# Optimization experiments

Measured on AMD Instinct MI355X. Metric: run time of the kernel, lower is better.

The kernel has to match this reference:

```python
import jax, jax.numpy as jnp
import numpy as np

PCH_SIZE = 8
STRIDE = 3


def setup_inputs() -> dict:
    key = jax.random.key(0)
    x = jax.random.normal(key, (8, 3, 512, 512), dtype=jnp.float32)
    return {"x": x}


def _estimate_noise(x, p=PCH_SIZE, s=STRIDE):
    B = x.shape[0]
    # Extract overlapping patches: [B, C*p*p, Hp, Wp] (NCHW input).
    pch = jax.lax.conv_general_dilated_patches(x, (p, p), (s, s), 'VALID')
    d = pch.shape[1]                       # C*p*p = 192
    pch = pch.reshape(B, d, -1)            # [B, d, num_pch]
    num_pch = pch.shape[-1]
    mu = pch.mean(axis=-1, keepdims=True)
    X = pch - mu
    # Patch covariance: [B, d, d]
    sigma_X = jnp.einsum('bdn,ben->bde', X, X) / num_pch
    sig = jnp.sort(jnp.linalg.eigvalsh(sigma_X), axis=-1)  # [B, d], ascending

    # Vectorized version of the original sequential threshold search.
    # Loop iteration ii = -1..-d uses prefix sig[..., :d+ii] of length L = d-1..0.
    ks = jnp.arange(d)
    L = d - 1 - ks                          # prefix lengths in original loop order
    csum = jnp.cumsum(sig, axis=-1)         # [B, d]
    prefix_sum = jnp.where(L > 0, csum[:, jnp.clip(L - 1, 0, d - 1)], 0.0)  # [B, d]
    tau = prefix_sum / jnp.maximum(L, 1).astype(sig.dtype)                  # [B, d]

    j = jnp.arange(d)
    in_prefix = j[None, :] < L[:, None]     # [K, d] membership of eig j in prefix k
    greater = (sig[:, None, :] > tau[:, :, None]) & in_prefix[None]
    less = (sig[:, None, :] < tau[:, :, None]) & in_prefix[None]
    valid = greater.sum(axis=-1) == less.sum(axis=-1)  # [B, K]

    # First valid iteration in loop order (mirrors the `found` flag).
    idx = jnp.argmax(valid, axis=-1)                    # [B]
    tau_sel = jnp.take_along_axis(tau, idx[:, None], axis=-1)[:, 0]
    return jnp.sqrt(tau_sel)                             # [B]


def reference(x):
    return _estimate_noise(x)
```

## Files before the change

kernel.cpp:

```cpp
#include <hip/hip_runtime.h>
#include <math.h>

#define NB 8
#define NC 3
#define PD 192
#define IMG 512
#define NP 169
#define NPATCH 28561
#define INV_N (1.0f/28561.0f)
#define KST 32

typedef float f4 __attribute__((ext_vector_type(4)));
typedef __bf16 bf16x8 __attribute__((ext_vector_type(8)));
typedef float f32x4 __attribute__((ext_vector_type(4)));

__device__ __forceinline__ float rdlane(float v, int lane) {
  return __uint_as_float(__builtin_amdgcn_readlane(__float_as_uint(v), lane));
}

template<int CTRL, int RM, int BM>
__device__ __forceinline__ float dpp_add(float x) {
  int sh = __builtin_amdgcn_update_dpp(0, __float_as_int(x), CTRL, RM, BM, false);
  return x + __int_as_float(sh);
}
__device__ __forceinline__ float wave_sum(float x) {
  x = dpp_add<0x111, 0xF, 0xF>(x);
  x = dpp_add<0x112, 0xF, 0xF>(x);
  x = dpp_add<0x114, 0xF, 0xF>(x);
  x = dpp_add<0x118, 0xF, 0xF>(x);
  x = dpp_add<0x142, 0xA, 0xF>(x);
  x = dpp_add<0x143, 0xC, 0xF>(x);
  return rdlane(x, 63);
}
__device__ __forceinline__ float row16_sum(float x) {
  x = dpp_add<0x111, 0xF, 0xF>(x);
  x = dpp_add<0x112, 0xF, 0xF>(x);
  x = dpp_add<0x114, 0xF, 0xF>(x);
  x = dpp_add<0x118, 0xF, 0xF>(x);
  return rdlane(x, 15);
}

__device__ __forceinline__ unsigned bfh(float v) {
  unsigned u = __float_as_uint(v);
  return (u + 0x7FFFu + ((u >> 16) & 1u)) >> 16;
}

__global__ __launch_bounds__(512) void cov_gemm_k(const float* __restrict__ x,
                                                  float* __restrict__ partial,
                                                  float* __restrict__ Spart,
                                                  int CH, int chunkSize) {
  int chunk = blockIdx.x % CH;
  int b = blockIdx.x / CH;
  int p0 = chunk * chunkSize;
  int pcount = NPATCH - p0;
  if (pcount > chunkSize) pcount = chunkSize;
  if (pcount < 0) pcount = 0;
  int nkt = (pcount + KST - 1) / KST;
  int pend = p0 + pcount;

  __shared__ unsigned short hiT[PD * 40];
  __shared__ unsigned short loT[PD * 40];
  __shared__ float sred[PD * 16];

  int t = threadIdx.x;
  int l = t & 63, w = t >> 6;
  int wr = w >> 2, wc = w & 3;
  int m0 = wr * 96, n0 = wc * 48;
  const float* imgb = x + (size_t)b * NC * IMG * IMG;

  f32x4 acc[6][3];
#pragma unroll
  for (int i = 0; i < 6; ++i)
#pragma unroll
    for (int j = 0; j < 3; ++j)
      acc[i][j] = (f32x4){0.f, 0.f, 0.f, 0.f};

  float fsum[6] = {0.f, 0.f, 0.f, 0.f, 0.f, 0.f};

  int krow = (l >> 4) << 3;
  int rsel = l & 15;

  for (int kt = 0; kt < nkt; ++kt) {
    int pbase = p0 + kt * KST;
#pragma unroll
    for (int s = 0; s < 6; ++s) {
      int idx = (s << 9) + t;
      int f = idx >> 4, p2 = idx & 15;
      int c = f >> 6, ii = (f >> 3) & 7, jj = f & 7;
      const float* imgc = imgb + (size_t)c * IMG * IMG;
      int P0 = pbase + (p2 << 1);
      float v0 = 0.f, v1 = 0.f;
      if (P0 < pend) { int ph = P0 / NP, pw = P0 - ph * NP; v0 = imgc[(3 * ph + ii) * IMG + 3 * pw + jj]; }
      if (P0 + 1 < pend) { int ph = (P0 + 1) / NP, pw = (P0 + 1) - ph * NP; v1 = imgc[(3 * ph + ii) * IMG + 3 * pw + jj]; }
      fsum[s] += v0 + v1;
      unsigned h0 = bfh(v0), h1 = bfh(v1);
      float r0 = v0 - __uint_as_float(h0 << 16);
      float r1 = v1 - __uint_as_float(h1 << 16);
      unsigned g0 = bfh(r0), g1 = bfh(r1);
      *(unsigned*)&hiT[f * 40 + (p2 << 1)] = h0 | (h1 << 16);
      *(unsigned*)&loT[f * 40 + (p2 << 1)] = g0 | (g1 << 16);
    }
    __syncthreads();

    bf16x8 ah[6], al[6], bh[3], bl[3];
#pragma unroll
    for (int i = 0; i < 6; ++i) {
      int row = m0 + i * 16 + rsel;
      ah[i] = *(const bf16x8*)&hiT[row * 40 + krow];
      al[i] = *(const bf16x8*)&loT[row * 40 + krow];
    }
#pragma unroll
    for (int j = 0; j < 3; ++j) {
      int row = n0 + j * 16 + rsel;
      bh[j] = *(const bf16x8*)&hiT[row * 40 + krow];
      bl[j] = *(const bf16x8*)&loT[row * 40 + krow];
    }
#pragma unroll
    for (int i = 0; i < 6; ++i)
#pragma unroll
      for (int j = 0; j < 3; ++j) {
        acc[i][j] = __builtin_amdgcn_mfma_f32_16x16x32_bf16(ah[i], bh[j], acc[i][j], 0, 0, 0);
        acc[i][j] = __builtin_amdgcn_mfma_f32_16x16x32_bf16(ah[i], bl[j], acc[i][j], 0, 0, 0);
        acc[i][j] = __builtin_amdgcn_mfma_f32_16x16x32_bf16(al[i], bh[j], acc[i][j], 0, 0, 0);
      }
    __syncthreads();
  }

#pragma unroll
  for (int s = 0; s < 6; ++s) {
    int f = (t >> 4) + (s << 5);
    sred[(f << 4) | (t & 15)] = fsum[s];
  }
  __syncthreads();
  if (t < PD) {
    float s = 0.f;
#pragma unroll
    for (int p2 = 0; p2 < 16; ++p2) s += sred[(t << 4) | p2];
    Spart[((size_t)chunk * NB + b) * PD + t] = s;
  }

  float* outp = partial + ((size_t)chunk * NB + b) * PD * PD;
#pragma unroll
  for (int i = 0; i < 6; ++i) {
    int rowb = m0 + i * 16 + ((l >> 4) << 2);
#pragma unroll
    for (int r = 0; r < 4; ++r)
#pragma unroll
      for (int j = 0; j < 3; ++j)
        outp[(size_t)(rowb + r) * PD + n0 + j * 16 + (l & 15)] = acc[i][j][r];
  }
}

__global__ __launch_bounds__(192) void musum_k(const float* __restrict__ Spart,
                                               float* __restrict__ S, int CH) {
  int b = blockIdx.x, t = threadIdx.x;
  float s = 0.f;
  for (int c = 0; c < CH; ++c) s += Spart[((size_t)c * NB + b) * PD + t];
  S[b * PD + t] = s;
}

__global__ __launch_bounds__(256) void reduce_fin_k(const float* __restrict__ partial,
                                                    const float* __restrict__ S,
                                                    float* __restrict__ G, int CH) {
  int e = blockIdx.x * 256 + threadIdx.x;
  const int tot = NB * PD * PD;
  if (e >= tot) return;
  int b = e / (PD * PD);
  int rem = e - b * PD * PD;
  int i = rem / PD, j = rem - i * PD;
  float s = 0.f;
  for (int c = 0; c < CH; ++c) s += partial[((size_t)c * NB + b) * PD * PD + rem];
  float mui = S[b * PD + i] * INV_N, muj = S[b * PD + j] * INV_N;
  G[e] = s * INV_N - mui * muj;
}

__global__ __launch_bounds__(384, 1) void eigen_k(const float* __restrict__ sigma,
                                                  float* __restrict__ out) {
  __shared__ float ppt[PD][12];
  __shared__ float vvg[2][PD];
  __shared__ float wvg[PD];
  __shared__ float red0[2];
  __shared__ float red2[16];
  __shared__ float dd[PD], ee[PD], e2[PD];
  __shared__ float sig[PD], csum[PD];
  __shared__ float grd[8];
  __shared__ float scanw[4];
  __shared__ int   redi[4];
  __shared__ int   cntb[2][PD];

  int b = blockIdx.x, t = threadIdx.x;
  int w = t >> 6, l = t & 63;
  int colbase = w << 5;
  const float* M = sigma + (size_t)b * PD * PD;

  f4 a[3][8];
#pragma unroll
  for (int rr = 0; rr < 3; ++rr) {
    const float* mp = M + (size_t)((rr << 6) + l) * PD + colbase;
#pragma unroll
    for (int cc = 0; cc < 8; ++cc)
      a[rr][cc] = *(const f4*)(mp + (cc << 2));
  }
  if (t >= 6 && t < 16) red2[t] = 0.f;
  if (t < PD) { ppt[t][6] = 0.f; ppt[t][7] = 0.f; }

  auto extract = [&](int c, float* av) {
#pragma unroll
    for (int cc = 0; cc < 8; ++cc)
#pragma unroll
      for (int e = 0; e < 4; ++e)
        if (colbase + (cc << 2) + e == c) {
          av[0] = a[0][cc][e]; av[1] = a[1][cc][e]; av[2] = a[2][cc][e];
        }
  };

  auto prep_core = [&](int c, float av0, float av1, float av2) {
    int k1 = c + 1;
    float am0 = (l >= k1) ? av0 : 0.f;
    float am1 = (l + 64 >= k1) ? av1 : 0.f;
    float am2 = (l + 128 >= k1) ? av2 : 0.f;
    float sq = wave_sum(am0 * am0 + am1 * am1 + am2 * am2);
    int slot2 = k1 >> 6;
    float tmp = (slot2 == 0) ? av0 : (slot2 == 1) ? av1 : av2;
    float x0 = rdlane(tmp, k1 & 63);
    float nrm = __builtin_amdgcn_sqrtf(sq);
    float alpha = (x0 >= 0.f) ? -nrm : nrm;
    bool degen = (sq < 1e-32f);
    float beta = degen ? 0.f : __builtin_amdgcn_rcpf(sq - alpha * x0);
    if (l == 0) {
      red0[c & 1] = beta;
      ee[c] = degen ? x0 : alpha;
    }
    float head = x0 - alpha;
    vvg[c & 1][l]       = (l       < k1) ? 0.f : (l       == k1) ? head : am0;
    vvg[c & 1][l + 64]  = (l + 64  < k1) ? 0.f : (l + 64  == k1) ? head : am1;
    vvg[c & 1][l + 128] = (l + 128 < k1) ? 0.f : (l + 128 == k1) ? head : am2;
  };

  if (w == 0) {
    float av[3] = {0.f, 0.f, 0.f};
    extract(0, av);
    prep_core(0, av[0], av[1], av[2]);
  }
  __syncthreads();

  for (int k = 0; k < PD - 2; ++k) {
    int cur = k & 1;
    int k1 = k + 1;
    bool wact = (colbase + 31) >= k1;

    float vr[3] = {0.f, 0.f, 0.f};
    f4 sv4[8];

    int sc0 = (w + (l >> 3)) % 6;
    int sc1 = (w + 8 + (l >> 3)) % 6;
    int sc2 = (w + 16 + (l >> 3)) % 6;

    if (wact) {
      vr[0] = vvg[cur][l]; vr[1] = vvg[cur][l + 64]; vr[2] = vvg[cur][l + 128];
#pragma unroll
      for (int cc = 0; cc < 8; ++cc)
        sv4[cc] = *(const f4*)&vvg[cur][colbase + (cc << 2)];
      float dp = 0.f;
#pragma unroll
      for (int rr = 0; rr < 3; ++rr) {
        if ((rr << 6) + 63 >= k1) {
          f4 s4 = sv4[0] * a[rr][0] + sv4[1] * a[rr][1]
                + sv4[2] * a[rr][2] + sv4[3] * a[rr][3]
                + sv4[4] * a[rr][4] + sv4[5] * a[rr][5]
                + sv4[6] * a[rr][6] + sv4[7] * a[rr][7];
          float s = (s4.x + s4.y) + (s4.z + s4.w);
          int sc = (rr == 0) ? sc0 : (rr == 1) ? sc1 : sc2;
          ppt[(rr << 6) + l][sc] = s;
          dp += vr[rr] * s;
        }
      }
      float dpt = wave_sum(dp);
      if (l == 0) red2[w] = dpt;
    } else if (k1 == colbase + 32) {
      ppt[l][sc0] = 0.f; ppt[l + 64][sc1] = 0.f; ppt[l + 128][sc2] = 0.f;
      if (l == 0) red2[w] = 0.f;
    }
    __syncthreads();

    if (wact) {
      float rv = red2[l & 15];
      float vt = row16_sum(rv);
      float beta = red0[cur];
      float Kc = 0.5f * beta * beta * vt;
      float wr[3] = {0.f, 0.f, 0.f};
#pragma unroll
      for (int rr = 0; rr < 3; ++rr) {
        if ((rr << 6) + 63 >= k1) {
          int row = (rr << 6) + l;
          f4 q = *(const f4*)&ppt[row][0];
          f4 q1 = *(const f4*)&ppt[row][4];
          q += q1;
          float p = (q.x + q.y) + (q.z + q.w);
          wr[rr] = (row >= k1) ? (beta * p - Kc * vr[rr]) : 0.f;
          wvg[row] = wr[rr];
        }
      }
      f4 sw4[8];
#pragma unroll
      for (int cc = 0; cc < 8; ++cc)
        sw4[cc] = *(const f4*)&wvg[colbase + (cc << 2)];
      int cn = k + 1;
      if (w == (cn >> 5)) {
        float av[3] = {0.f, 0.f, 0.f};
        extract(cn, av);
        float svv = vvg[cur][cn];
        float swv = wvg[cn];
#pragma unroll
        for (int rr = 0; rr < 3; ++rr) av[rr] -= vr[rr] * swv + wr[rr] * svv;
        prep_core(cn, av[0], av[1], av[2]);
      }
#pragma unroll
      for (int rr = 0; rr < 3; ++rr) {
        if ((rr << 6) + 63 >= k1) {
          float vrr = vr[rr], wrr = wr[rr];
#pragma unroll
          for (int cc = 0; cc < 8; ++cc)
            a[rr][cc] -= sw4[cc] * vrr + sv4[cc] * wrr;
        }
      }
    }
    __syncthreads();
  }

#pragma unroll
  for (int rr = 0; rr < 3; ++rr) {
    int row = (rr << 6) + l;
#pragma unroll
    for (int cc = 0; cc < 8; ++cc)
#pragma unroll
      for (int e = 0; e < 4; ++e)
        if (colbase + (cc << 2) + e == row) dd[row] = a[rr][cc][e];
  }
  __syncthreads();

  if (t < PD - 1) e2[t] = ee[t] * ee[t];

  float glo = 1e30f, ghi = -1e30f;
  if (t < PD) {
    float r = 0.f;
    if (t > 0) r += fabsf(ee[t - 1]);
    if (t < PD - 1) r += fabsf(ee[t]);
    glo = dd[t] - r;
    ghi = dd[t] + r;
  }
#pragma unroll
  for (int off = 32; off; off >>= 1) {
    glo = fminf(glo, __shfl_xor(glo, off, 64));
    ghi = fmaxf(ghi, __shfl_xor(ghi, off, 64));
  }
  if (l == 0 && w < 3) { grd[w] = glo; grd[4 + w] = ghi; }
  __syncthreads();
  float gl = fminf(grd[0], fminf(grd[1], grd[2]));
  float gh = fmaxf(grd[4], fmaxf(grd[5], grd[6]));
  float wid = gh - gl;
  gl -= 1e-3f * wid + 1e-20f;
  gh += 1e-3f * wid + 1e-20f;

  {
    int sub = (t >= PD) ? 1 : 0;
    int e = t - PD * sub;
    float lo = gl, hi = gh;
    for (int round = 0; round < 10; ++round) {
      float width = hi - lo;
      float xm = lo + width * ((sub == 0) ? 0.333333343f : 0.666666687f);
      int cnt = 0;
      float q = 1.0f;
      for (int i = 0; i < PD; ++i) {
        float term = (i > 0) ? e2[i - 1] * __builtin_amdgcn_rcpf(q) : 0.0f;
        q = (dd[i] - xm) - term;
        cnt += (q < 0.f);
        float aq = fabsf(q);
        if (aq < 1e-30f) q = (q < 0.f) ? -1e-30f : 1e-30f;
      }
      cntb[sub][e] = cnt;
      __syncthreads();
      int c0 = cntb[0][e], c1 = cntb[1][e];
      float mA = lo + width * 0.333333343f;
      float mB = lo + width * 0.666666687f;
      float nl = lo, nh = hi;
      if (c0 <= e) nl = mA;
      if (c1 <= e) nl = mB;
      if (c1 > e) nh = mB;
      if (c0 > e) nh = mA;
      lo = nl; hi = nh;
      __syncthreads();
    }
    if (sub == 0) sig[e] = 0.5f * (lo + hi);
  }
  __syncthreads();

  {
    float x = (t < PD) ? sig[t] : 0.f;
    float scn = x;
#pragma unroll
    for (int off = 1; off < 64; off <<= 1) {
      float u = __shfl_up(scn, off, 64);
      if (l >= off) scn += u;
    }
    if (l == 63 && w < 3) scanw[w] = scn;
    __syncthreads();
    if (t < PD) {
      float base = 0.f;
      if (w >= 1) base += scanw[0];
      if (w >= 2) base += scanw[1];
      csum[t] = scn + base;
    }
  }
  __syncthreads();

  float tau = 0.f;
  int vk = 1 << 30;
  if (t < PD) {
    int L = PD - 1 - t;
    tau = (L > 0) ? csum[L - 1] / (float)L : 0.0f;
    int gt = 0, lt2 = 0;
    for (int j = 0; j < L; ++j) {
      float svv = sig[j];
      gt  += (svv > tau);
      lt2 += (svv < tau);
    }
    if (gt == lt2) vk = t;
  }
#pragma unroll
  for (int off = 32; off; off >>= 1) vk = min(vk, __shfl_xor(vk, off, 64));
  if (l == 0 && w < 3) redi[w] = vk;
  __syncthreads();
  if (t == 0) {
    int g = min(redi[0], min(redi[1], redi[2]));
    redi[3] = (g == (1 << 30)) ? 0 : g;
  }
  __syncthreads();
  if (t < PD && t == redi[3]) out[b] = sqrtf(fmaxf(tau, 0.f));
}

extern "C" void kernel_launch(void* const* d_in, const int* in_sizes, int n_in,
                              void* d_out, int out_size, void* d_ws, size_t ws_size,
                              hipStream_t stream) {
  const float* x = (const float*)d_in[0];
  float* out = (float*)d_out;

  size_t gElems = (size_t)NB * PD * PD;
  int CH = 32;
  while (CH > 1 &&
         ws_size < ((size_t)CH + 1) * gElems * 4 + (size_t)NB * PD * 4 +
                   (size_t)CH * NB * PD * 4)
    CH >>= 1;
  float* G = (float*)d_ws;
  float* partial = G + gElems;
  float* S = partial + (size_t)CH * gElems;
  float* Spart = S + (size_t)NB * PD;
  int chunkSize = (NPATCH + CH - 1) / CH;

  cov_gemm_k<<<NB * CH, 512, 0, stream>>>(x, partial, Spart, CH, chunkSize);
  musum_k<<<NB, 192, 0, stream>>>(Spart, S, CH);
  reduce_fin_k<<<(int)((gElems + 255) / 256), 256, 0, stream>>>(partial, S, G, CH);
  eigen_k<<<NB, 384, 0, stream>>>(G, out);
}
```

Measured before the change: 501.8 us.

## Split tridiagonalization columns across eight waves of 24 instead of six of 32

```diff
diff --git a/kernel.cpp b/kernel.cpp
--- a/kernel.cpp
+++ b/kernel.cpp
@@ -9,6 +9,7 @@
 #define NPATCH 28561
 #define INV_N (1.0f/28561.0f)
 #define KST 32
+#define CB2 24
 
 typedef float f4 __attribute__((ext_vector_type(4)));
 typedef __bf16 bf16x8 __attribute__((ext_vector_type(8)));
@@ -174,7 +175,7 @@
   G[e] = s * INV_N - mui * muj;
 }
 
-__global__ __launch_bounds__(384, 1) void eigen_k(const float* __restrict__ sigma,
+__global__ __launch_bounds__(512, 1) void eigen_k(const float* __restrict__ sigma,
                                                   float* __restrict__ out) {
   __shared__ float ppt[PD][12];
   __shared__ float vvg[2][PD];
@@ -190,23 +191,22 @@
 
   int b = blockIdx.x, t = threadIdx.x;
   int w = t >> 6, l = t & 63;
-  int colbase = w << 5;
+  int colbase = w * CB2;
   const float* M = sigma + (size_t)b * PD * PD;
 
-  f4 a[3][8];
+  f4 a[3][6];
 #pragma unroll
   for (int rr = 0; rr < 3; ++rr) {
     const float* mp = M + (size_t)((rr << 6) + l) * PD + colbase;
 #pragma unroll
-    for (int cc = 0; cc < 8; ++cc)
+    for (int cc = 0; cc < 6; ++cc)
       a[rr][cc] = *(const f4*)(mp + (cc << 2));
   }
-  if (t >= 6 && t < 16) red2[t] = 0.f;
-  if (t < PD) { ppt[t][6] = 0.f; ppt[t][7] = 0.f; }
+  if (t >= 8 && t < 16) red2[t] = 0.f;
 
   auto extract = [&](int c, float* av) {
 #pragma unroll
-    for (int cc = 0; cc < 8; ++cc)
+    for (int cc = 0; cc < 6; ++cc)
 #pragma unroll
       for (int e = 0; e < 4; ++e)
         if (colbase + (cc << 2) + e == c) {
@@ -247,38 +247,31 @@
   for (int k = 0; k < PD - 2; ++k) {
     int cur = k & 1;
     int k1 = k + 1;
-    bool wact = (colbase + 31) >= k1;
+    bool wact = (colbase + CB2 - 1) >= k1;
 
     float vr[3] = {0.f, 0.f, 0.f};
-    f4 sv4[8];
-
-    int sc0 = (w + (l >> 3)) % 6;
-    int sc1 = (w + 8 + (l >> 3)) % 6;
-    int sc2 = (w + 16 + (l >> 3)) % 6;
+    f4 sv4[6];
 
     if (wact) {
       vr[0] = vvg[cur][l]; vr[1] = vvg[cur][l + 64]; vr[2] = vvg[cur][l + 128];
 #pragma unroll
-      for (int cc = 0; cc < 8; ++cc)
+      for (int cc = 0; cc < 6; ++cc)
         sv4[cc] = *(const f4*)&vvg[cur][colbase + (cc << 2)];
       float dp = 0.f;
 #pragma unroll
       for (int rr = 0; rr < 3; ++rr) {
         if ((rr << 6) + 63 >= k1) {
-          f4 s4 = sv4[0] * a[rr][0] + sv4[1] * a[rr][1]
-                + sv4[2] * a[rr][2] + sv4[3] * a[rr][3]
-                + sv4[4] * a[rr][4] + sv4[5] * a[rr][5]
-                + sv4[6] * a[rr][6] + sv4[7] * a[rr][7];
+          f4 s4 = sv4[0] * a[rr][0] + sv4[1] * a[rr][1] + sv4[2] * a[rr][2]
+                + sv4[3] * a[rr][3] + sv4[4] * a[rr][4] + sv4[5] * a[rr][5];
           float s = (s4.x + s4.y) + (s4.z + s4.w);
-          int sc = (rr == 0) ? sc0 : (rr == 1) ? sc1 : sc2;
-          ppt[(rr << 6) + l][sc] = s;
+          ppt[(rr << 6) + l][w] = s;
           dp += vr[rr] * s;
         }
       }
       float dpt = wave_sum(dp);
       if (l == 0) red2[w] = dpt;
-    } else if (k1 == colbase + 32) {
-      ppt[l][sc0] = 0.f; ppt[l + 64][sc1] = 0.f; ppt[l + 128][sc2] = 0.f;
+    } else if (k1 == colbase + CB2) {
+      ppt[l][w] = 0.f; ppt[l + 64][w] = 0.f; ppt[l + 128][w] = 0.f;
       if (l == 0) red2[w] = 0.f;
     }
     __syncthreads();
@@ -298,15 +291,16 @@
           q += q1;
           float p = (q.x + q.y) + (q.z + q.w);
           wr[rr] = (row >= k1) ? (beta * p - Kc * vr[rr]) : 0.f;
-          wvg[row] = wr[rr];
+          if (row >= colbase && row < colbase + CB2)
+            wvg[row] = wr[rr];
         }
       }
-      f4 sw4[8];
-#pragma unroll
-      for (int cc = 0; cc < 8; ++cc)
+      f4 sw4[6];
+#pragma unroll
+      for (int cc = 0; cc < 6; ++cc)
         sw4[cc] = *(const f4*)&wvg[colbase + (cc << 2)];
       int cn = k + 1;
-      if (w == (cn >> 5)) {
+      if (w == cn / CB2) {
         float av[3] = {0.f, 0.f, 0.f};
         extract(cn, av);
         float svv = vvg[cur][cn];
@@ -320,7 +314,7 @@
         if ((rr << 6) + 63 >= k1) {
           float vrr = vr[rr], wrr = wr[rr];
 #pragma unroll
-          for (int cc = 0; cc < 8; ++cc)
+          for (int cc = 0; cc < 6; ++cc)
             a[rr][cc] -= sw4[cc] * vrr + sv4[cc] * wrr;
         }
       }
@@ -332,7 +326,7 @@
   for (int rr = 0; rr < 3; ++rr) {
     int row = (rr << 6) + l;
 #pragma unroll
-    for (int cc = 0; cc < 8; ++cc)
+    for (int cc = 0; cc < 6; ++cc)
 #pragma unroll
       for (int e = 0; e < 4; ++e)
         if (colbase + (cc << 2) + e == row) dd[row] = a[rr][cc][e];
@@ -363,35 +357,41 @@
   gh += 1e-3f * wid + 1e-20f;
 
   {
-    int sub = (t >= PD) ? 1 : 0;
-    int e = t - PD * sub;
+    bool act = t < 2 * PD;
+    int sub = 0, e = 0;
+    if (act) { sub = (t >= PD) ? 1 : 0; e = t - PD * sub; }
     float lo = gl, hi = gh;
     for (int round = 0; round < 10; ++round) {
-      float width = hi - lo;
-      float xm = lo + width * ((sub == 0) ? 0.333333343f : 0.666666687f);
-      int cnt = 0;
-      float q = 1.0f;
-      for (int i = 0; i < PD; ++i) {
-        float term = (i > 0) ? e2[i - 1] * __builtin_amdgcn_rcpf(q) : 0.0f;
-        q = (dd[i] - xm) - term;
-        cnt += (q < 0.f);
-        float aq = fabsf(q);
-        if (aq < 1e-30f) q = (q < 0.f) ? -1e-30f : 1e-30f;
-      }
-      cntb[sub][e] = cnt;
+      if (act) {
+        float width = hi - lo;
+        float xm = lo + width * ((sub == 0) ? 0.333333343f : 0.666666687f);
+        int cnt = 0;
+        float q = 1.0f;
+        for (int i = 0; i < PD; ++i) {
+          float term = (i > 0) ? e2[i - 1] * __builtin_amdgcn_rcpf(q) : 0.0f;
+          q = (dd[i] - xm) - term;
+          cnt += (q < 0.f);
+          float aq = fabsf(q);
+          if (aq < 1e-30f) q = (q < 0.f) ? -1e-30f : 1e-30f;
+        }
+        cntb[sub][e] = cnt;
+      }
       __syncthreads();
-      int c0 = cntb[0][e], c1 = cntb[1][e];
-      float mA = lo + width * 0.333333343f;
-      float mB = lo + width * 0.666666687f;
-      float nl = lo, nh = hi;
-      if (c0 <= e) nl = mA;
-      if (c1 <= e) nl = mB;
-      if (c1 > e) nh = mB;
-      if (c0 > e) nh = mA;
-      lo = nl; hi = nh;
+      if (act) {
+        int c0 = cntb[0][e], c1 = cntb[1][e];
+        float width = hi - lo;
+        float mA = lo + width * 0.333333343f;
+        float mB = lo + width * 0.666666687f;
+        float nl = lo, nh = hi;
+        if (c0 <= e) nl = mA;
+        if (c1 <= e) nl = mB;
+        if (c1 > e) nh = mB;
+        if (c0 > e) nh = mA;
+        lo = nl; hi = nh;
+      }
       __syncthreads();
     }
-    if (sub == 0) sig[e] = 0.5f * (lo + hi);
+    if (act && sub == 0) sig[e] = 0.5f * (lo + hi);
   }
   __syncthreads();
 
@@ -460,5 +460,5 @@
   cov_gemm_k<<<NB * CH, 512, 0, stream>>>(x, partial, Spart, CH, chunkSize);
   musum_k<<<NB, 192, 0, stream>>>(Spart, S, CH);
   reduce_fin_k<<<(int)((gElems + 255) / 256), 256, 0, stream>>>(partial, S, G, CH);
-  eigen_k<<<NB, 384, 0, stream>>>(G, out);
-}
+  eigen_k<<<NB, 512, 0, stream>>>(G, out);
+}
```

Measured after the change: 483.7 us. -3.6%, faster.
